# Kernel optimization log

Measured on AMD Instinct MI355X. Metric: run time of the kernel, lower is better.

The kernel has to match this reference:

```python
import jax, jax.numpy as jnp
import numpy as np

B, IN, H = 16384, 512, 512


def setup_inputs() -> dict:
    key = jax.random.key(0)
    ks = jax.random.split(key, 7)
    s_in = 1.0 / np.sqrt(IN)
    s_h = 1.0 / np.sqrt(H)
    return {
        "x": jax.random.normal(ks[0], (B, IN), jnp.float32),
        "h": jax.random.normal(ks[1], (B, H), jnp.float32),
        "c": jax.random.normal(ks[2], (B, H), jnp.float32),
        # packed gate weights, order [i, f, g, o] along last dim (4*H)
        "Wx": jax.random.normal(ks[3], (IN, 4 * H), jnp.float32) * s_in,
        "Wh": jax.random.normal(ks[4], (H, 4 * H), jnp.float32) * s_h,
        "bx": jax.random.normal(ks[5], (4 * H,), jnp.float32) * s_in,
        "bh": jax.random.normal(ks[6], (4 * H,), jnp.float32) * s_h,
    }


def reference(x, h, c, Wx, Wh, bx, bh):
    # one fused GEMM per input stream instead of 8 small linears; same math
    gates = x @ Wx + bx + h @ Wh + bh          # [B, 4H]
    gi, gf, gg, go = jnp.split(gates, 4, axis=-1)
    i = jax.nn.sigmoid(gi)
    f = jax.nn.sigmoid(gf)
    g = jnp.tanh(gg)
    o = jax.nn.sigmoid(go)
    c_new = f * c + i * g
    h_new = o * jnp.tanh(c_new)
    return (h_new, c_new)
```

## Files before the change

kernel.cpp:

```cpp
#include <hip/hip_runtime.h>
#include <hip/hip_bf16.h>

#define B_DIM   16384
#define IN_DIM  512
#define H_DIM   512
#define K_DIM   1024
#define N4H     2048
#define BH      (B_DIM * H_DIM)

typedef __attribute__((ext_vector_type(8))) short  short8;
typedef __attribute__((ext_vector_type(4))) short  short4v;
typedef __attribute__((ext_vector_type(4))) float  f32x4;

__device__ inline void async_load16(const void* g, void* l) {
    __builtin_amdgcn_global_load_lds(
        (const __attribute__((address_space(1))) void*)g,
        (__attribute__((address_space(3)))       void*)l, 16, 0, 0);
}

__device__ inline short bf16bits(float f) {
    __hip_bfloat16 b = __float2bfloat16(f);
    return *reinterpret_cast<short*>(&b);
}

__device__ inline float sigmoidf_(float v) {
    return 1.0f / (1.0f + __expf(-v));
}
__device__ inline float tanhf_(float v) {
    v = fminf(fmaxf(v, -30.f), 30.f);
    float e = __expf(2.f * v);
    return (e - 1.f) / (e + 1.f);
}

__global__ __launch_bounds__(256) void prep_weights(
    const float* __restrict__ Wx, const float* __restrict__ Wh,
    const float* __restrict__ bx, const float* __restrict__ bh,
    __hip_bfloat16* __restrict__ Wt, float* __restrict__ bias_p) {
    __shared__ __hip_bfloat16 tile[32][33];
    const int bid = blockIdx.x;
    const int bk  = bid & 31;
    const int bn  = bid >> 5;
    const int t   = threadIdx.x;
    const int kb  = bk * 32, nb = bn * 32;

#pragma unroll
    for (int r = 0; r < 4; ++r) {
        int k_loc = r * 8 + (t >> 5);
        int n_loc = t & 31;
        int kg = kb + k_loc;
        float v = (kg < IN_DIM) ? Wx[(size_t)kg * N4H + nb + n_loc]
                                : Wh[(size_t)(kg - IN_DIM) * N4H + nb + n_loc];
        tile[k_loc][n_loc] = __float2bfloat16(v);
    }
    __syncthreads();

    {
        int n_loc = t >> 3;
        int k_loc = (t & 7) * 4;
        int ng = nb + n_loc;
        int g  = ng >> 9;
        int c  = ng & 511;
        int row_out = (c >> 5) * 128 + g * 32 + (c & 31);
        short4v v4;
        v4.x = *reinterpret_cast<short*>(&tile[k_loc + 0][n_loc]);
        v4.y = *reinterpret_cast<short*>(&tile[k_loc + 1][n_loc]);
        v4.z = *reinterpret_cast<short*>(&tile[k_loc + 2][n_loc]);
        v4.w = *reinterpret_cast<short*>(&tile[k_loc + 3][n_loc]);
        *(short4v*)&Wt[(size_t)row_out * K_DIM + kb + k_loc] = v4;
    }

    if (bid < 8) {
        int ng = bid * 256 + t;
        int g  = ng >> 9;
        int c  = ng & 511;
        int ro = (c >> 5) * 128 + g * 32 + (c & 31);
        bias_p[ro] = bx[ng] + bh[ng];
    }
}

__global__ __launch_bounds__(256, 3) void lstm_gemm(
    const float* __restrict__ x, const float* __restrict__ h,
    const float* __restrict__ c_in,
    const __hip_bfloat16* __restrict__ Wt, const float* __restrict__ bias_p,
    float* __restrict__ out) {
    __shared__ __hip_bfloat16 lds_a[128 * 32];
    __shared__ __hip_bfloat16 lds_b[128 * 32];

    const int tid   = threadIdx.x;
    const int bn    = blockIdx.x & 15;
    const int bm    = blockIdx.x >> 4;
    const int w     = tid >> 6;
    const int lane  = tid & 63;
    const int col16 = lane & 15;
    const int quad  = lane >> 4;

    f32x4 acc[2][8];
#pragma unroll
    for (int mi = 0; mi < 2; ++mi)
#pragma unroll
        for (int ni = 0; ni < 8; ++ni)
            acc[mi][ni] = (f32x4){0.f, 0.f, 0.f, 0.f};

    const __hip_bfloat16* wt_base = Wt + (size_t)(bn * 128) * K_DIM;

    const int chunk0 = w * 2;
    const int e0     = chunk0 * 512 + lane * 8;
    const int bn_loc0 = e0 >> 5, bk_off0 = e0 & 31;
    const int e1     = (chunk0 + 1) * 512 + lane * 8;
    const int bn_loc1 = e1 >> 5, bk_off1 = e1 & 31;

    for (int kt = 0; kt < 32; ++kt) {
        const int kb = kt * 32;
        const float* aptr;
        int koff;
        if (kb < IN_DIM) { aptr = x; koff = kb; }
        else             { aptr = h; koff = kb - IN_DIM; }

        async_load16(wt_base + (size_t)bn_loc0 * K_DIM + kb + bk_off0,
                     (void*)(lds_b + chunk0 * 512));
        async_load16(wt_base + (size_t)bn_loc1 * K_DIM + kb + bk_off1,
                     (void*)(lds_b + (chunk0 + 1) * 512));

        float4 av[4];
#pragma unroll
        for (int j = 0; j < 4; ++j) {
            int cch = j * 256 + tid;
            int row = cch >> 3;
            int kq  = (cch & 7) * 4;
            av[j] = *(const float4*)(aptr + (size_t)(bm * 128 + row) * IN_DIM
                                     + koff + kq);
        }
#pragma unroll
        for (int j = 0; j < 4; ++j) {
            int cch = j * 256 + tid;
            int row = cch >> 3;
            int kq  = (cch & 7) * 4;
            short4v sv;
            sv.x = bf16bits(av[j].x);
            sv.y = bf16bits(av[j].y);
            sv.z = bf16bits(av[j].z);
            sv.w = bf16bits(av[j].w);
            *(short4v*)&lds_a[row * 32 + kq] = sv;
        }
        __syncthreads();

        short8 afr[2], bfr[8];
#pragma unroll
        for (int mi = 0; mi < 2; ++mi)
            afr[mi] = *(const short8*)&lds_a[(w * 32 + mi * 16 + col16) * 32 + quad * 8];
#pragma unroll
        for (int ni = 0; ni < 8; ++ni)
            bfr[ni] = *(const short8*)&lds_b[(ni * 16 + col16) * 32 + quad * 8];
#pragma unroll
        for (int mi = 0; mi < 2; ++mi)
#pragma unroll
            for (int ni = 0; ni < 8; ++ni)
                acc[mi][ni] = __builtin_amdgcn_mfma_f32_16x16x32_bf16(
                    afr[mi], bfr[ni], acc[mi][ni], 0, 0, 0);
        __syncthreads();
    }

    float bias_v[4][2];
#pragma unroll
    for (int g = 0; g < 4; ++g)
#pragma unroll
        for (int h2 = 0; h2 < 2; ++h2)
            bias_v[g][h2] = bias_p[bn * 128 + g * 32 + h2 * 16 + col16];

#pragma unroll
    for (int mi = 0; mi < 2; ++mi) {
#pragma unroll
        for (int reg = 0; reg < 4; ++reg) {
            const int m_g = bm * 128 + w * 32 + mi * 16 + quad * 4 + reg;
#pragma unroll
            for (int h2 = 0; h2 < 2; ++h2) {
                const int hc_g = bn * 32 + h2 * 16 + col16;
                float gi = acc[mi][0 + h2][reg] + bias_v[0][h2];
                float gf = acc[mi][2 + h2][reg] + bias_v[1][h2];
                float gg = acc[mi][4 + h2][reg] + bias_v[2][h2];
                float go = acc[mi][6 + h2][reg] + bias_v[3][h2];
                float iv = sigmoidf_(gi);
                float fv = sigmoidf_(gf);
                float gv = tanhf_(gg);
                float ov = sigmoidf_(go);
                float co = c_in[(size_t)m_g * H_DIM + hc_g];
                float cn = fv * co + iv * gv;
                float hn = ov * tanhf_(cn);
                out[(size_t)m_g * H_DIM + hc_g]      = hn;
                out[BH + (size_t)m_g * H_DIM + hc_g] = cn;
            }
        }
    }
}

extern "C" void kernel_launch(void* const* d_in, const int* in_sizes, int n_in,
                              void* d_out, int out_size, void* d_ws, size_t ws_size,
                              hipStream_t stream) {
    const float* x  = (const float*)d_in[0];
    const float* h  = (const float*)d_in[1];
    const float* c  = (const float*)d_in[2];
    const float* Wx = (const float*)d_in[3];
    const float* Wh = (const float*)d_in[4];
    const float* bx = (const float*)d_in[5];
    const float* bh = (const float*)d_in[6];

    __hip_bfloat16* Wt = (__hip_bfloat16*)d_ws;
    float* bias_p = (float*)((char*)d_ws + (size_t)N4H * K_DIM * 2);

    prep_weights<<<2048, 256, 0, stream>>>(Wx, Wh, bx, bh, Wt, bias_p);
    lstm_gemm<<<2048, 256, 0, stream>>>(x, h, c, Wt, bias_p, (float*)d_out);
}
```

Before: 256.9 us.

## Pre-convert x/h to bf16 and stream both GEMM operands asynchronously into LDS

```diff
diff --git a/kernel.cpp b/kernel.cpp
--- a/kernel.cpp
+++ b/kernel.cpp
@@ -32,68 +32,91 @@
     return (e - 1.f) / (e + 1.f);
 }
 
-__global__ __launch_bounds__(256) void prep_weights(
+__global__ __launch_bounds__(256) void prep_all(
     const float* __restrict__ Wx, const float* __restrict__ Wh,
     const float* __restrict__ bx, const float* __restrict__ bh,
-    __hip_bfloat16* __restrict__ Wt, float* __restrict__ bias_p) {
-    __shared__ __hip_bfloat16 tile[32][33];
+    const float* __restrict__ x,  const float* __restrict__ h,
+    __hip_bfloat16* __restrict__ Wt, __hip_bfloat16* __restrict__ Axh,
+    float* __restrict__ bias_p) {
     const int bid = blockIdx.x;
-    const int bk  = bid & 31;
-    const int bn  = bid >> 5;
     const int t   = threadIdx.x;
-    const int kb  = bk * 32, nb = bn * 32;
-
-#pragma unroll
-    for (int r = 0; r < 4; ++r) {
-        int k_loc = r * 8 + (t >> 5);
-        int n_loc = t & 31;
-        int kg = kb + k_loc;
-        float v = (kg < IN_DIM) ? Wx[(size_t)kg * N4H + nb + n_loc]
-                                : Wh[(size_t)(kg - IN_DIM) * N4H + nb + n_loc];
-        tile[k_loc][n_loc] = __float2bfloat16(v);
-    }
-    __syncthreads();
-
-    {
-        int n_loc = t >> 3;
-        int k_loc = (t & 7) * 4;
-        int ng = nb + n_loc;
-        int g  = ng >> 9;
-        int c  = ng & 511;
-        int row_out = (c >> 5) * 128 + g * 32 + (c & 31);
-        short4v v4;
-        v4.x = *reinterpret_cast<short*>(&tile[k_loc + 0][n_loc]);
-        v4.y = *reinterpret_cast<short*>(&tile[k_loc + 1][n_loc]);
-        v4.z = *reinterpret_cast<short*>(&tile[k_loc + 2][n_loc]);
-        v4.w = *reinterpret_cast<short*>(&tile[k_loc + 3][n_loc]);
-        *(short4v*)&Wt[(size_t)row_out * K_DIM + kb + k_loc] = v4;
-    }
-
-    if (bid < 8) {
-        int ng = bid * 256 + t;
-        int g  = ng >> 9;
-        int c  = ng & 511;
-        int ro = (c >> 5) * 128 + g * 32 + (c & 31);
-        bias_p[ro] = bx[ng] + bh[ng];
+
+    if (bid < 2048) {
+        __shared__ __hip_bfloat16 tile[32][33];
+        const int bk = bid & 31;
+        const int bn = bid >> 5;
+        const int kb = bk * 32, nb = bn * 32;
+#pragma unroll
+        for (int r = 0; r < 4; ++r) {
+            int k_loc = r * 8 + (t >> 5);
+            int n_loc = t & 31;
+            int kg = kb + k_loc;
+            float v = (kg < IN_DIM) ? Wx[(size_t)kg * N4H + nb + n_loc]
+                                    : Wh[(size_t)(kg - IN_DIM) * N4H + nb + n_loc];
+            tile[k_loc][n_loc] = __float2bfloat16(v);
+        }
+        __syncthreads();
+        {
+            int n_loc = t >> 3;
+            int k_loc = (t & 7) * 4;
+            int ng = nb + n_loc;
+            int g  = ng >> 9;
+            int c  = ng & 511;
+            int row_out = (c >> 5) * 128 + g * 32 + (c & 31);
+            short4v v4;
+            v4.x = *reinterpret_cast<short*>(&tile[k_loc + 0][n_loc]);
+            v4.y = *reinterpret_cast<short*>(&tile[k_loc + 1][n_loc]);
+            v4.z = *reinterpret_cast<short*>(&tile[k_loc + 2][n_loc]);
+            v4.w = *reinterpret_cast<short*>(&tile[k_loc + 3][n_loc]);
+            *(short4v*)&Wt[(size_t)row_out * K_DIM + kb + k_loc] = v4;
+        }
+        if (bid < 8) {
+            int ng = bid * 256 + t;
+            int g  = ng >> 9;
+            int c  = ng & 511;
+            int ro = (c >> 5) * 128 + g * 32 + (c & 31);
+            bias_p[ro] = bx[ng] + bh[ng];
+        }
+    } else {
+        const int ab = bid - 2048;
+        const int kq = t;
+        const float* src = (kq < 128) ? (x + kq * 4)
+                                      : (h + (size_t)(kq - 128) * 4);
+#pragma unroll
+        for (int j = 0; j < 8; ++j) {
+            int m = ab * 8 + j;
+            float4 v = *(const float4*)(src + (size_t)m * 512);
+            short4v sv;
+            sv.x = bf16bits(v.x);
+            sv.y = bf16bits(v.y);
+            sv.z = bf16bits(v.z);
+            sv.w = bf16bits(v.w);
+            *(short4v*)&Axh[(size_t)m * K_DIM + kq * 4] = sv;
+        }
     }
 }
 
 __global__ __launch_bounds__(256, 3) void lstm_gemm(
-    const float* __restrict__ x, const float* __restrict__ h,
     const float* __restrict__ c_in,
-    const __hip_bfloat16* __restrict__ Wt, const float* __restrict__ bias_p,
+    const __hip_bfloat16* __restrict__ Axh,
+    const __hip_bfloat16* __restrict__ Wt,
+    const float* __restrict__ bias_p,
     float* __restrict__ out) {
     __shared__ __hip_bfloat16 lds_a[128 * 32];
     __shared__ __hip_bfloat16 lds_b[128 * 32];
 
     const int tid   = threadIdx.x;
-    const int bn    = blockIdx.x & 15;
-    const int bm    = blockIdx.x >> 4;
     const int w     = tid >> 6;
     const int lane  = tid & 63;
     const int col16 = lane & 15;
     const int quad  = lane >> 4;
 
+    const int jb    = blockIdx.x;
+    const int xcd   = jb & 7;
+    const int local = jb >> 3;
+    const int bm    = xcd * 16 + (local >> 4);
+    const int bn    = local & 15;
+
     f32x4 acc[2][8];
 #pragma unroll
     for (int mi = 0; mi < 2; ++mi)
@@ -101,56 +124,50 @@
         for (int ni = 0; ni < 8; ++ni)
             acc[mi][ni] = (f32x4){0.f, 0.f, 0.f, 0.f};
 
-    const __hip_bfloat16* wt_base = Wt + (size_t)(bn * 128) * K_DIM;
-
-    const int chunk0 = w * 2;
-    const int e0     = chunk0 * 512 + lane * 8;
-    const int bn_loc0 = e0 >> 5, bk_off0 = e0 & 31;
-    const int e1     = (chunk0 + 1) * 512 + lane * 8;
-    const int bn_loc1 = e1 >> 5, bk_off1 = e1 & 31;
+    const __hip_bfloat16* Ab = Axh + (size_t)bm * 128 * K_DIM;
+    const __hip_bfloat16* Bb = Wt  + (size_t)bn * 128 * K_DIM;
+
+    const int s0 = w * 128 + lane;
+    const int s1 = s0 + 64;
+    const int r0 = s0 >> 2, r1 = s1 >> 2;
+    const int q0 = ((s0 & 3) - ((r0 >> 1) & 3)) & 3;
+    const int q1 = ((s1 & 3) - ((r1 >> 1) & 3)) & 3;
+    const size_t ga0 = (size_t)r0 * K_DIM + q0 * 8;
+    const size_t ga1 = (size_t)r1 * K_DIM + q1 * 8;
+    __hip_bfloat16* la0 = lds_a + w * 1024;
+    __hip_bfloat16* la1 = lds_a + w * 1024 + 512;
+    __hip_bfloat16* lb0 = lds_b + w * 1024;
+    __hip_bfloat16* lb1 = lds_b + w * 1024 + 512;
+
+    int aoff[2], boff[8];
+#pragma unroll
+    for (int mi = 0; mi < 2; ++mi) {
+        int r = w * 32 + mi * 16 + col16;
+        aoff[mi] = (r * 4 + ((quad + ((r >> 1) & 3)) & 3)) * 16;
+    }
+#pragma unroll
+    for (int ni = 0; ni < 8; ++ni) {
+        int r = ni * 16 + col16;
+        boff[ni] = (r * 4 + ((quad + ((r >> 1) & 3)) & 3)) * 16;
+    }
+    const char* lap = (const char*)lds_a;
+    const char* lbp = (const char*)lds_b;
 
     for (int kt = 0; kt < 32; ++kt) {
         const int kb = kt * 32;
-        const float* aptr;
-        int koff;
-        if (kb < IN_DIM) { aptr = x; koff = kb; }
-        else             { aptr = h; koff = kb - IN_DIM; }
-
-        async_load16(wt_base + (size_t)bn_loc0 * K_DIM + kb + bk_off0,
-                     (void*)(lds_b + chunk0 * 512));
-        async_load16(wt_base + (size_t)bn_loc1 * K_DIM + kb + bk_off1,
-                     (void*)(lds_b + (chunk0 + 1) * 512));
-
-        float4 av[4];
-#pragma unroll
-        for (int j = 0; j < 4; ++j) {
-            int cch = j * 256 + tid;
-            int row = cch >> 3;
-            int kq  = (cch & 7) * 4;
-            av[j] = *(const float4*)(aptr + (size_t)(bm * 128 + row) * IN_DIM
-                                     + koff + kq);
-        }
-#pragma unroll
-        for (int j = 0; j < 4; ++j) {
-            int cch = j * 256 + tid;
-            int row = cch >> 3;
-            int kq  = (cch & 7) * 4;
-            short4v sv;
-            sv.x = bf16bits(av[j].x);
-            sv.y = bf16bits(av[j].y);
-            sv.z = bf16bits(av[j].z);
-            sv.w = bf16bits(av[j].w);
-            *(short4v*)&lds_a[row * 32 + kq] = sv;
-        }
+        async_load16(Ab + ga0 + kb, la0);
+        async_load16(Ab + ga1 + kb, la1);
+        async_load16(Bb + ga0 + kb, lb0);
+        async_load16(Bb + ga1 + kb, lb1);
         __syncthreads();
 
         short8 afr[2], bfr[8];
 #pragma unroll
         for (int mi = 0; mi < 2; ++mi)
-            afr[mi] = *(const short8*)&lds_a[(w * 32 + mi * 16 + col16) * 32 + quad * 8];
+            afr[mi] = *(const short8*)(lap + aoff[mi]);
 #pragma unroll
         for (int ni = 0; ni < 8; ++ni)
-            bfr[ni] = *(const short8*)&lds_b[(ni * 16 + col16) * 32 + quad * 8];
+            bfr[ni] = *(const short8*)(lbp + boff[ni]);
 #pragma unroll
         for (int mi = 0; mi < 2; ++mi)
 #pragma unroll
@@ -193,6 +210,154 @@
     }
 }
 
+__global__ __launch_bounds__(256) void prep_weights_fb(
+    const float* __restrict__ Wx, const float* __restrict__ Wh,
+    const float* __restrict__ bx, const float* __restrict__ bh,
+    __hip_bfloat16* __restrict__ Wt, float* __restrict__ bias_p) {
+    __shared__ __hip_bfloat16 tile[32][33];
+    const int bid = blockIdx.x;
+    const int bk  = bid & 31;
+    const int bn  = bid >> 5;
+    const int t   = threadIdx.x;
+    const int kb  = bk * 32, nb = bn * 32;
+#pragma unroll
+    for (int r = 0; r < 4; ++r) {
+        int k_loc = r * 8 + (t >> 5);
+        int n_loc = t & 31;
+        int kg = kb + k_loc;
+        float v = (kg < IN_DIM) ? Wx[(size_t)kg * N4H + nb + n_loc]
+                                : Wh[(size_t)(kg - IN_DIM) * N4H + nb + n_loc];
+        tile[k_loc][n_loc] = __float2bfloat16(v);
+    }
+    __syncthreads();
+    {
+        int n_loc = t >> 3;
+        int k_loc = (t & 7) * 4;
+        int ng = nb + n_loc;
+        int g  = ng >> 9;
+        int c  = ng & 511;
+        int row_out = (c >> 5) * 128 + g * 32 + (c & 31);
+        short4v v4;
+        v4.x = *reinterpret_cast<short*>(&tile[k_loc + 0][n_loc]);
+        v4.y = *reinterpret_cast<short*>(&tile[k_loc + 1][n_loc]);
+        v4.z = *reinterpret_cast<short*>(&tile[k_loc + 2][n_loc]);
+        v4.w = *reinterpret_cast<short*>(&tile[k_loc + 3][n_loc]);
+        *(short4v*)&Wt[(size_t)row_out * K_DIM + kb + k_loc] = v4;
+    }
+    if (bid < 8) {
+        int ng = bid * 256 + t;
+        int g  = ng >> 9;
+        int c  = ng & 511;
+        int ro = (c >> 5) * 128 + g * 32 + (c & 31);
+        bias_p[ro] = bx[ng] + bh[ng];
+    }
+}
+
+__global__ __launch_bounds__(256, 3) void lstm_gemm_fb(
+    const float* __restrict__ x, const float* __restrict__ h,
+    const float* __restrict__ c_in,
+    const __hip_bfloat16* __restrict__ Wt, const float* __restrict__ bias_p,
+    float* __restrict__ out) {
+    __shared__ __hip_bfloat16 lds_a[128 * 32];
+    __shared__ __hip_bfloat16 lds_b[128 * 32];
+    const int tid   = threadIdx.x;
+    const int bn    = blockIdx.x & 15;
+    const int bm    = blockIdx.x >> 4;
+    const int w     = tid >> 6;
+    const int lane  = tid & 63;
+    const int col16 = lane & 15;
+    const int quad  = lane >> 4;
+    f32x4 acc[2][8];
+#pragma unroll
+    for (int mi = 0; mi < 2; ++mi)
+#pragma unroll
+        for (int ni = 0; ni < 8; ++ni)
+            acc[mi][ni] = (f32x4){0.f, 0.f, 0.f, 0.f};
+    const __hip_bfloat16* wt_base = Wt + (size_t)(bn * 128) * K_DIM;
+    const int chunk0 = w * 2;
+    const int e0     = chunk0 * 512 + lane * 8;
+    const int bn_loc0 = e0 >> 5, bk_off0 = e0 & 31;
+    const int e1     = (chunk0 + 1) * 512 + lane * 8;
+    const int bn_loc1 = e1 >> 5, bk_off1 = e1 & 31;
+    for (int kt = 0; kt < 32; ++kt) {
+        const int kb = kt * 32;
+        const float* aptr;
+        int koff;
+        if (kb < IN_DIM) { aptr = x; koff = kb; }
+        else             { aptr = h; koff = kb - IN_DIM; }
+        async_load16(wt_base + (size_t)bn_loc0 * K_DIM + kb + bk_off0,
+                     (void*)(lds_b + chunk0 * 512));
+        async_load16(wt_base + (size_t)bn_loc1 * K_DIM + kb + bk_off1,
+                     (void*)(lds_b + (chunk0 + 1) * 512));
+        float4 av[4];
+#pragma unroll
+        for (int j = 0; j < 4; ++j) {
+            int cch = j * 256 + tid;
+            int row = cch >> 3;
+            int kq  = (cch & 7) * 4;
+            av[j] = *(const float4*)(aptr + (size_t)(bm * 128 + row) * IN_DIM
+                                     + koff + kq);
+        }
+#pragma unroll
+        for (int j = 0; j < 4; ++j) {
+            int cch = j * 256 + tid;
+            int row = cch >> 3;
+            int kq  = (cch & 7) * 4;
+            short4v sv;
+            sv.x = bf16bits(av[j].x);
+            sv.y = bf16bits(av[j].y);
+            sv.z = bf16bits(av[j].z);
+            sv.w = bf16bits(av[j].w);
+            *(short4v*)&lds_a[row * 32 + kq] = sv;
+        }
+        __syncthreads();
+        short8 afr[2], bfr[8];
+#pragma unroll
+        for (int mi = 0; mi < 2; ++mi)
+            afr[mi] = *(const short8*)&lds_a[(w * 32 + mi * 16 + col16) * 32 + quad * 8];
+#pragma unroll
+        for (int ni = 0; ni < 8; ++ni)
+            bfr[ni] = *(const short8*)&lds_b[(ni * 16 + col16) * 32 + quad * 8];
+#pragma unroll
+        for (int mi = 0; mi < 2; ++mi)
+#pragma unroll
+            for (int ni = 0; ni < 8; ++ni)
+                acc[mi][ni] = __builtin_amdgcn_mfma_f32_16x16x32_bf16(
+                    afr[mi], bfr[ni], acc[mi][ni], 0, 0, 0);
+        __syncthreads();
+    }
+    float bias_v[4][2];
+#pragma unroll
+    for (int g = 0; g < 4; ++g)
+#pragma unroll
+        for (int h2 = 0; h2 < 2; ++h2)
+            bias_v[g][h2] = bias_p[bn * 128 + g * 32 + h2 * 16 + col16];
+#pragma unroll
+    for (int mi = 0; mi < 2; ++mi) {
+#pragma unroll
+        for (int reg = 0; reg < 4; ++reg) {
+            const int m_g = bm * 128 + w * 32 + mi * 16 + quad * 4 + reg;
+#pragma unroll
+            for (int h2 = 0; h2 < 2; ++h2) {
+                const int hc_g = bn * 32 + h2 * 16 + col16;
+                float gi = acc[mi][0 + h2][reg] + bias_v[0][h2];
+                float gf = acc[mi][2 + h2][reg] + bias_v[1][h2];
+                float gg = acc[mi][4 + h2][reg] + bias_v[2][h2];
+                float go = acc[mi][6 + h2][reg] + bias_v[3][h2];
+                float iv = sigmoidf_(gi);
+                float fv = sigmoidf_(gf);
+                float gv = tanhf_(gg);
+                float ov = sigmoidf_(go);
+                float co = c_in[(size_t)m_g * H_DIM + hc_g];
+                float cn = fv * co + iv * gv;
+                float hn = ov * tanhf_(cn);
+                out[(size_t)m_g * H_DIM + hc_g]      = hn;
+                out[BH + (size_t)m_g * H_DIM + hc_g] = cn;
+            }
+        }
+    }
+}
+
 extern "C" void kernel_launch(void* const* d_in, const int* in_sizes, int n_in,
                               void* d_out, int out_size, void* d_ws, size_t ws_size,
                               hipStream_t stream) {
@@ -204,9 +369,20 @@
     const float* bx = (const float*)d_in[5];
     const float* bh = (const float*)d_in[6];
 
-    __hip_bfloat16* Wt = (__hip_bfloat16*)d_ws;
-    float* bias_p = (float*)((char*)d_ws + (size_t)N4H * K_DIM * 2);
-
-    prep_weights<<<2048, 256, 0, stream>>>(Wx, Wh, bx, bh, Wt, bias_p);
-    lstm_gemm<<<2048, 256, 0, stream>>>(x, h, c, Wt, bias_p, (float*)d_out);
-}
+    const size_t wtBytes  = (size_t)N4H * K_DIM * 2;
+    const size_t axhBytes = (size_t)B_DIM * K_DIM * 2;
+    const size_t need     = wtBytes + axhBytes + (size_t)N4H * 4;
+
+    if (ws_size >= need) {
+        __hip_bfloat16* Wt  = (__hip_bfloat16*)d_ws;
+        __hip_bfloat16* Axh = (__hip_bfloat16*)((char*)d_ws + wtBytes);
+        float* bias_p = (float*)((char*)d_ws + wtBytes + axhBytes);
+        prep_all<<<4096, 256, 0, stream>>>(Wx, Wh, bx, bh, x, h, Wt, Axh, bias_p);
+        lstm_gemm<<<2048, 256, 0, stream>>>(c, Axh, Wt, bias_p, (float*)d_out);
+    } else {
+        __hip_bfloat16* Wt = (__hip_bfloat16*)d_ws;
+        float* bias_p = (float*)((char*)d_ws + wtBytes);
+        prep_weights_fb<<<2048, 256, 0, stream>>>(Wx, Wh, bx, bh, Wt, bias_p);
+        lstm_gemm_fb<<<2048, 256, 0, stream>>>(x, h, c, Wt, bias_p, (float*)d_out);
+    }
+}
```

Result: faster. 250.8 us (-2.4%).
